# Kernel tuning notes

Hardware: AMD Instinct MI355X
Metric: run time of the kernel (lower is better)

## Reference

```python
import jax, jax.numpy as jnp
import numpy as np

D_MODEL = 256
D_INNER = 512
NHEADS = 8
HEADDIM = 64
NGROUPS = 1
D_DIST = 4
LOG_SCALE = 512.0
MAX_VALUE = 4.0
NUM_POINTS = 10
EPS = 1e-5


def roty(t):
    c, s = jnp.cos(t), jnp.sin(t)
    z, o = jnp.zeros_like(t), jnp.ones_like(t)
    r0 = jnp.stack([c, z, s], -1)
    r1 = jnp.stack([z, o, z], -1)
    r2 = jnp.stack([-s, z, c], -1)
    return jnp.stack([r0, r1, r2], -2)


def box_corners(center, size, angle):
    # flip_axis_to_camera: (x, -z, y)
    cam_c = jnp.stack([center[..., 0], -center[..., 2], center[..., 1]], -1)
    R = roty(angle)  # (B,K,3,3)
    sx = jnp.array([1, 1, -1, -1, 1, 1, -1, -1], jnp.float32)
    sy = jnp.array([1, 1, 1, 1, -1, -1, -1, -1], jnp.float32)
    sz = jnp.array([1, -1, -1, 1, 1, -1, -1, 1], jnp.float32)
    l, w, h = size[..., 0:1], size[..., 1:2], size[..., 2:3]
    local = jnp.stack([l * sx / 2, h * sy / 2, w * sz / 2], -1)  # (B,K,8,3)
    cam = jnp.einsum('bkcj,bkij->bkci', local, R) + cam_c[..., None, :]
    # camera -> lidar: (x, z, -y)
    return jnp.stack([cam[..., 0], cam[..., 2], -cam[..., 1]], -1)


def trilinear_sample(table, g):
    # table (P,P,P,C); g (N,3) normalized coords (gx,gy,gz); gx->axis2, gy->axis1, gz->axis0
    # replicates F.grid_sample(mode='bilinear', align_corners=False, padding_mode='zeros')
    P = table.shape[0]
    pix = ((g + 1.0) * P - 1.0) * 0.5
    k, j, i = pix[:, 0], pix[:, 1], pix[:, 2]
    i0f, j0f, k0f = jnp.floor(i), jnp.floor(j), jnp.floor(k)
    wi, wj, wk = i - i0f, j - j0f, k - k0f
    i0, j0, k0 = i0f.astype(jnp.int32), j0f.astype(jnp.int32), k0f.astype(jnp.int32)
    out = jnp.zeros((g.shape[0], table.shape[-1]), table.dtype)
    for a in (0, 1):
        for b in (0, 1):
            for c in (0, 1):
                ii, jj, kk = i0 + a, j0 + b, k0 + c
                valid = (ii >= 0) & (ii < P) & (jj >= 0) & (jj < P) & (kk >= 0) & (kk < P)
                v = table[jnp.clip(ii, 0, P - 1), jnp.clip(jj, 0, P - 1), jnp.clip(kk, 0, P - 1)]
                w = (wi if a else 1 - wi) * (wj if b else 1 - wj) * (wk if c else 1 - wk)
                out = out + jnp.where(valid, w, 0.0)[:, None] * v
    return out


def box_dist(key_xyz, query_xyz, query_size, query_angle, w1, b1, w2):
    B, K = query_xyz.shape[:2]
    L = key_xyz.shape[1]
    corners = jax.lax.stop_gradient(box_corners(query_xyz, query_size, query_angle))
    d = corners.reshape(B, K * 8, 3)[:, :, None, :] - key_xyz[:, None, :, :]  # (B,K*8,L,3)
    d = jnp.stack([d[..., 0], -d[..., 2], d[..., 1]], -1)
    R = roty(jnp.tile(query_angle, (1, 8)))  # matches torch .repeat((1,8)) ordering (bug-faithful)
    d = jnp.einsum('bqlj,bqjk->bqlk', d, R)
    d = jnp.stack([d[..., 0], d[..., 2], -d[..., 1]], -1)
    d = jnp.sign(d) * jnp.log2(jnp.abs(d) * LOG_SCALE + 1.0) / np.float32(np.log2(8.0))
    g = (d / MAX_VALUE).reshape(-1, 3)
    lin = jnp.linspace(-MAX_VALUE, MAX_VALUE, NUM_POINTS, dtype=jnp.float32)
    coords = jnp.stack(jnp.meshgrid(lin, lin, lin, indexing='ij'), -1)  # (P,P,P,3)
    table = jnp.maximum(coords @ w1.T + b1, 0.0) @ w2.T  # cpb MLP -> (P,P,P,4)
    samp = trilinear_sample(table, g).reshape(B, K, 8, L, D_DIST)
    return samp.sum(axis=2).transpose(0, 2, 1, 3)  # (B,L,K,4)


def dwconv7(x, w, b):
    # x (B,L,C), depthwise conv1d k=7 pad=3
    y = jax.lax.conv_general_dilated(jnp.swapaxes(x, 1, 2), w, (1,), [(3, 3)],
                                     dimension_numbers=('NCH', 'OIH', 'NCH'),
                                     feature_group_count=w.shape[0])
    return jnp.swapaxes(y + b[None, :, None], 1, 2)


def issm_scan(x, Bm, Cm, dt, A, h0):
    # x (B,L,H,hd), Bm/Cm (B,L,K), dt (B,L,K,H), h0 (B,H,hd,K); state index = query axis K
    dA = jnp.exp(dt * A)          # (B,L,K,H)
    dB = dt * Bm[..., None]       # (B,L,K,H)
    xs = (jnp.moveaxis(x, 1, 0), jnp.moveaxis(dA, 1, 0), jnp.moveaxis(dB, 1, 0), jnp.moveaxis(Cm, 1, 0))

    def step(h, inp):
        x_t, dA_t, dB_t, C_t = inp
        h = h * jnp.swapaxes(dA_t, 1, 2)[:, :, None, :] + x_t[..., None] * jnp.swapaxes(dB_t, 1, 2)[:, :, None, :]
        return h, jnp.einsum('bhdk,bk->bhd', h, C_t)

    hT, ys = jax.lax.scan(step, h0, xs)
    return jnp.moveaxis(ys, 0, 1), hT


def _forward(in_key, in_query, key_xyz, query_xyz, query_size, query_angle, Wkey, conv_w, conv_b, convb_w, convb_b, Wq, Wbc, Wdt, dt_bias, A_log, Dp, Wok, Woq, key_norm_w, ln_w, ln_b, cpb_w1, cpb_b1, cpb_w2):
    B, L, _ = in_key.shape
    K = in_query.shape[1]
    zxbcdt = in_key @ Wkey.T
    z = zxbcdt[..., :D_INNER]
    xbc = zxbcdt[..., D_INNER:2 * D_INNER + 2 * NGROUPS]
    dt_k = zxbcdt[..., 2 * D_INNER + 2 * NGROUPS:]
    xbc_f = jax.nn.silu(dwconv7(xbc, conv_w, conv_b))
    x = xbc_f[..., :D_INNER].reshape(B, L, NHEADS, HEADDIM)
    b_bias = xbc_f[..., D_INNER:D_INNER + NGROUPS]
    c_bias = xbc_f[..., D_INNER + NGROUPS:]
    xbc_b = jax.nn.silu(dwconv7(xbc_f, convb_w, convb_b))
    x_b = xbc_b[..., :D_INNER].reshape(B, L, NHEADS, HEADDIM)
    bb_b = xbc_b[..., D_INNER:D_INNER + NGROUPS]
    cb_b = xbc_b[..., D_INNER + NGROUPS:]
    dist = box_dist(key_xyz, query_xyz, query_size, query_angle, cpb_w1, cpb_b1, cpb_w2)  # (B,L,K,4)
    bc = dist @ Wbc.T  # (B,L,K,2*ngroups)
    Bm0, Cm0 = bc[..., 0], bc[..., 1]
    dt = jax.nn.softplus(dist @ Wdt.T + dt_k[:, :, None, :] + dt_bias)  # (B,L,K,H)
    A = -jnp.exp(A_log)
    h0 = (in_query @ Wq.T).reshape(B, K, NHEADS, HEADDIM).transpose(0, 2, 3, 1)  # (B,H,hd,K)
    y_f, h_f = issm_scan(x, Bm0 + b_bias, Cm0 + c_bias, dt, A, h0)
    rev = lambda a: jnp.flip(a, axis=1)
    y_b, h_b = issm_scan(rev(x_b), rev(Bm0 + bb_b), rev(Cm0 + cb_b), rev(dt), A, h0)
    y = y_f + rev(y_b) + Dp[None, None, :, None] * x
    yk = y.reshape(B, L, D_INNER)
    gated = yk * jax.nn.silu(z)
    gated = gated * jax.lax.rsqrt(jnp.mean(gated * gated, -1, keepdims=True) + EPS) * key_norm_w
    out_key = gated @ Wok.T
    state = (0.5 * (h_f + h_b)).transpose(0, 3, 1, 2).reshape(B, K, D_INNER)
    mu = jnp.mean(state, -1, keepdims=True)
    var = jnp.mean((state - mu) ** 2, -1, keepdims=True)
    out_query = (((state - mu) * jax.lax.rsqrt(var + EPS)) * ln_w + ln_b) @ Woq.T
    return out_key, out_query


def setup_inputs():
    key = jax.random.key(0)
    ks = jax.random.split(key, 24)
    B, L, K = 2, 1024, 128
    D, DI, H, G = D_MODEL, D_INNER, NHEADS, NGROUPS
    CC = DI + 2 * G
    n = jax.random.normal
    inp = {}
    inp['in_key'] = n(ks[0], (B, L, D), jnp.float32)
    inp['in_query'] = n(ks[1], (B, K, D), jnp.float32)
    inp['key_xyz'] = jax.random.uniform(ks[2], (B, L, 3))
    inp['query_xyz'] = jax.random.uniform(ks[3], (B, K, 3))
    inp['query_size'] = jax.random.uniform(ks[4], (B, K, 3)) + 0.1
    inp['query_angle'] = jax.random.uniform(ks[5], (B, K)) * 2.0 * np.float32(np.pi)
    inp['Wkey'] = n(ks[6], (2 * DI + 2 * G + H, D)) * 0.02
    inp['conv_w'] = n(ks[7], (CC, 1, 7)) * 0.1
    inp['conv_b'] = jnp.zeros((CC,))
    inp['convb_w'] = n(ks[8], (CC, 1, 7)) * 0.1
    inp['convb_b'] = jnp.zeros((CC,))
    inp['Wq'] = n(ks[9], (DI, D)) * 0.02
    inp['Wbc'] = n(ks[10], (2 * G, D_DIST)) * 0.1
    inp['Wdt'] = n(ks[11], (H, D_DIST)) * 0.1
    dt = jnp.exp(jax.random.uniform(ks[12], (H,)) * (np.float32(np.log(0.1)) - np.float32(np.log(1e-4))) + np.float32(np.log(1e-4)))
    inp['dt_bias'] = dt + jnp.log(-jnp.expm1(-dt))
    inp['A_log'] = jnp.log(jax.random.uniform(ks[13], (H,), minval=1.0, maxval=16.0))
    inp['Dp'] = jnp.ones((H,))
    inp['Wok'] = n(ks[14], (D, DI)) * 0.02
    inp['Woq'] = n(ks[15], (D, DI)) * 0.02
    inp['key_norm_w'] = jnp.ones((DI,))
    inp['ln_w'] = jnp.ones((DI,))
    inp['ln_b'] = jnp.zeros((DI,))
    inp['cpb_w1'] = n(ks[16], (128, 3)) * 0.1
    inp['cpb_b1'] = jnp.zeros((128,))
    inp['cpb_w2'] = n(ks[17], (D_DIST, 128)) * 0.1
    return inp


def reference(in_key, in_query, key_xyz, query_xyz, query_size, query_angle, Wkey, conv_w, conv_b, convb_w, convb_b, Wq, Wbc, Wdt, dt_bias, A_log, Dp, Wok, Woq, key_norm_w, ln_w, ln_b, cpb_w1, cpb_b1, cpb_w2):
    return _forward(in_key, in_query, key_xyz, query_xyz, query_size, query_angle, Wkey, conv_w, conv_b, convb_w, convb_b, Wq, Wbc, Wdt, dt_bias, A_log, Dp, Wok, Woq, key_norm_w, ln_w, ln_b, cpb_w1, cpb_b1, cpb_w2)
```

## Files before the change

kernel.cpp:

```cpp
#include <hip/hip_runtime.h>
#include <math.h>

#define B_ 2
#define L_ 1024
#define K_ 128
#define DM 256
#define DI 512
#define NH 8
#define HD 64
#define CC 514
#define ZCOLS 1034
#define NC 16
#define TC 64

typedef __attribute__((ext_vector_type(8))) short bf16x8;
typedef __attribute__((ext_vector_type(4))) float f32x4;

__device__ __forceinline__ float wave_sum(float v) {
    v += __shfl_xor(v, 1);  v += __shfl_xor(v, 2);  v += __shfl_xor(v, 4);
    v += __shfl_xor(v, 8);  v += __shfl_xor(v, 16); v += __shfl_xor(v, 32);
    return v;
}

__device__ __forceinline__ float dpp_row_reduce16(float v) {
    int t;
    t = __builtin_amdgcn_update_dpp(0, __float_as_int(v), 0x128, 0xF, 0xF, true);
    v += __int_as_float(t);
    t = __builtin_amdgcn_update_dpp(0, __float_as_int(v), 0x124, 0xF, 0xF, true);
    v += __int_as_float(t);
    t = __builtin_amdgcn_update_dpp(0, __float_as_int(v), 0x122, 0xF, 0xF, true);
    v += __int_as_float(t);
    t = __builtin_amdgcn_update_dpp(0, __float_as_int(v), 0x121, 0xF, 0xF, true);
    v += __int_as_float(t);
    return v;
}

__device__ __forceinline__ float silu_f(float x) {
    return x / (1.f + expf(-x));
}

__device__ __forceinline__ unsigned short f2bf(float f) {
    unsigned u = __float_as_uint(f);
    u = (u + 0x7FFFu + ((u >> 16) & 1u)) >> 16;
    return (unsigned short)u;
}

__global__ __launch_bounds__(256) void cvt_k(
    const float* __restrict__ ik, const float* __restrict__ wk,
    const float* __restrict__ iq, const float* __restrict__ wq,
    const float* __restrict__ wok,
    unsigned short* __restrict__ ikb, unsigned short* __restrict__ wkb,
    unsigned short* __restrict__ iqb, unsigned short* __restrict__ wqb,
    unsigned short* __restrict__ wokb) {
    int i = blockIdx.x * 256 + threadIdx.x;
    float4 v;
    ushort4* dst;
    if (i < 131072) {
        v = ((const float4*)ik)[i];
        dst = ((ushort4*)ikb) + i;
    } else if (i < 200704) {
        int j = i - 131072;
        v = (j < 66176) ? ((const float4*)wk)[j] : make_float4(0.f, 0.f, 0.f, 0.f);
        dst = ((ushort4*)wkb) + j;
    } else if (i < 217088) {
        int j = i - 200704;
        v = ((const float4*)iq)[j];
        dst = ((ushort4*)iqb) + j;
    } else if (i < 249856) {
        int j = i - 217088;
        v = ((const float4*)wq)[j];
        dst = ((ushort4*)wqb) + j;
    } else if (i < 282624) {
        int j = i - 249856;
        v = ((const float4*)wok)[j];
        dst = ((ushort4*)wokb) + j;
    } else return;
    ushort4 o;
    o.x = f2bf(v.x); o.y = f2bf(v.y); o.z = f2bf(v.z); o.w = f2bf(v.w);
    *dst = o;
}

__device__ __forceinline__ void mfma_dev(
    const unsigned short* __restrict__ A, const unsigned short* __restrict__ B,
    float* __restrict__ C, int ldc, int K, int bm, int bn, int nmax) {
    int tid = threadIdx.x;
    int lane = tid & 63, wv = tid >> 6;
    int wm = wv >> 1, wn = wv & 1;
    int r = lane & 15, kg = lane >> 4;
    const unsigned short* A0 = A + (size_t)(bm + wm * 32 + r) * K + kg * 8;
    const unsigned short* A1 = A0 + 16 * K;
    const unsigned short* B0 = B + (size_t)(bn + wn * 32 + r) * K + kg * 8;
    const unsigned short* B1 = B0 + 16 * K;
    f32x4 acc00 = {0.f, 0.f, 0.f, 0.f}, acc01 = acc00, acc10 = acc00, acc11 = acc00;
#pragma unroll 4
    for (int k0 = 0; k0 < K; k0 += 32) {
        bf16x8 a0 = *(const bf16x8*)(A0 + k0);
        bf16x8 a1 = *(const bf16x8*)(A1 + k0);
        bf16x8 b0 = *(const bf16x8*)(B0 + k0);
        bf16x8 b1 = *(const bf16x8*)(B1 + k0);
        acc00 = __builtin_amdgcn_mfma_f32_16x16x32_bf16(a0, b0, acc00, 0, 0, 0);
        acc01 = __builtin_amdgcn_mfma_f32_16x16x32_bf16(a0, b1, acc01, 0, 0, 0);
        acc10 = __builtin_amdgcn_mfma_f32_16x16x32_bf16(a1, b0, acc10, 0, 0, 0);
        acc11 = __builtin_amdgcn_mfma_f32_16x16x32_bf16(a1, b1, acc11, 0, 0, 0);
    }
    int mb = bm + wm * 32, nb = bn + wn * 32;
#pragma unroll
    for (int j = 0; j < 4; ++j) {
        int m0 = mb + kg * 4 + j;
        int n0 = nb + r;
        if (n0 < nmax)      C[(size_t)m0 * ldc + n0] = acc00[j];
        if (n0 + 16 < nmax) C[(size_t)m0 * ldc + n0 + 16] = acc01[j];
        int m1 = m0 + 16;
        if (n0 < nmax)      C[(size_t)m1 * ldc + n0] = acc10[j];
        if (n0 + 16 < nmax) C[(size_t)m1 * ldc + n0 + 16] = acc11[j];
    }
}

__global__ __launch_bounds__(256, 4) void front_k(
    const unsigned short* __restrict__ ikb, const unsigned short* __restrict__ wkb,
    const unsigned short* __restrict__ iqb, const unsigned short* __restrict__ wqb,
    const float* __restrict__ in_key, const float* __restrict__ Wkey,
    float* __restrict__ zx, float* __restrict__ h0b,
    const float* __restrict__ qxyz, const float* __restrict__ qsize,
    const float* __restrict__ qang, const float* __restrict__ w1,
    const float* __restrict__ b1, const float* __restrict__ w2,
    float* __restrict__ cb, float* __restrict__ tbl) {
    int bid = blockIdx.x, tid = threadIdx.x;
    if (bid < 544) {
        mfma_dev(ikb, wkb, zx, ZCOLS, 256, (bid & 31) * 64, (bid >> 5) * 64, 1026);
    } else if (bid < 576) {
        int rr = bid - 544;
        mfma_dev(iqb, wqb, h0b, 512, 256, (rr & 3) * 64, (rr >> 2) * 64, 512);
    } else if (bid < 584) {
        int idx = (bid - 576) * 256 + tid;
        int b = idx >> 10;
        int q = idx & 1023;
        int k = q >> 3;
        int c = q & 7;
        const float sx[8] = {1, 1, -1, -1, 1, 1, -1, -1};
        const float sy[8] = {1, 1, 1, 1, -1, -1, -1, -1};
        const float sz[8] = {1, -1, -1, 1, 1, -1, -1, 1};
        float cx = qxyz[(b * K_ + k) * 3 + 0];
        float cy = qxyz[(b * K_ + k) * 3 + 1];
        float cz = qxyz[(b * K_ + k) * 3 + 2];
        float lv = qsize[(b * K_ + k) * 3 + 0];
        float wv2 = qsize[(b * K_ + k) * 3 + 1];
        float hv = qsize[(b * K_ + k) * 3 + 2];
        float ang = qang[b * K_ + k];
        float ca = cosf(ang), sa = sinf(ang);
        float ccx = cx, ccy = -cz, ccz = cy;
        float l0 = lv * sx[c] * 0.5f;
        float l1 = hv * sy[c] * 0.5f;
        float l2 = wv2 * sz[c] * 0.5f;
        float m0 = ca * l0 + sa * l2 + ccx;
        float m1 = l1 + ccy;
        float m2 = -sa * l0 + ca * l2 + ccz;
        float angr = qang[b * K_ + (q & (K_ - 1))];
        float4* o = (float4*)(cb + (size_t)idx * 8);
        o[0] = make_float4(m0, m2, -m1, cosf(angr));
        o[1] = make_float4(sinf(angr), 0.f, 0.f, 0.f);
    } else if (bid < 588) {
        int p = (bid - 584) * 256 + tid;
        if (p >= 1000) return;
        int i = p / 100, j = (p / 10) % 10, k = p % 10;
        float c0 = (8.f / 9.f) * i - 4.f;
        float c1 = (8.f / 9.f) * j - 4.f;
        float c2 = (8.f / 9.f) * k - 4.f;
        float a0 = 0.f, a1 = 0.f, a2 = 0.f, a3 = 0.f;
        for (int m = 0; m < 128; ++m) {
            float t = fmaf(c0, w1[m * 3 + 0], fmaf(c1, w1[m * 3 + 1], fmaf(c2, w1[m * 3 + 2], b1[m])));
            t = fmaxf(t, 0.f);
            a0 = fmaf(t, w2[m], a0);
            a1 = fmaf(t, w2[128 + m], a1);
            a2 = fmaf(t, w2[256 + m], a2);
            a3 = fmaf(t, w2[384 + m], a3);
        }
        tbl[p * 4 + 0] = a0; tbl[p * 4 + 1] = a1;
        tbl[p * 4 + 2] = a2; tbl[p * 4 + 3] = a3;
    } else {
        int row = (bid - 588) * 32 + (tid >> 3);
        int colh = tid & 7;
        const float* arow = in_key + (size_t)row * 256;
        const float* wrow = Wkey + (size_t)(1026 + colh) * 256;
        float acc = 0.f;
#pragma unroll 8
        for (int k = 0; k < 256; k += 4) {
            float4 a = *(const float4*)(arow + k);
            float4 wv2 = *(const float4*)(wrow + k);
            acc = fmaf(a.x, wv2.x, fmaf(a.y, wv2.y, fmaf(a.z, wv2.z, fmaf(a.w, wv2.w, acc))));
        }
        zx[(size_t)row * ZCOLS + 1026 + colh] = acc;
    }
}

__global__ void dwconv_silu(const float* __restrict__ xin, int in_stride, int in_off,
                            const float* __restrict__ w, const float* __restrict__ bias,
                            float* __restrict__ out) {
    int c = blockIdx.y * blockDim.x + threadIdx.x;
    if (c >= CC) return;
    int row0 = blockIdx.x * 2;
    int l0 = row0 & (L_ - 1);
    const float* xr = xin + (size_t)row0 * in_stride + in_off + c;
    float Lv[8];
#pragma unroll
    for (int i = 0; i < 8; ++i) {
        int ll = l0 + i - 3;
        Lv[i] = (ll >= 0 && ll < L_) ? xr[(ptrdiff_t)(i - 3) * in_stride] : 0.f;
    }
    float acc0 = bias[c], acc1 = bias[c];
#pragma unroll
    for (int j = 0; j < 7; ++j) {
        float wj = w[c * 7 + j];
        acc0 = fmaf(Lv[j], wj, acc0);
        acc1 = fmaf(Lv[j + 1], wj, acc1);
    }
    out[(size_t)row0 * CC + c] = silu_f(acc0);
    out[(size_t)(row0 + 1) * CC + c] = silu_f(acc1);
}

__global__ __launch_bounds__(128) void geo_k(
    const float* __restrict__ kxyz, const float* __restrict__ cb,
    const float* __restrict__ tbl, const float* __restrict__ zx,
    const float* __restrict__ xf, const float* __restrict__ xb,
    const float* __restrict__ wbc, const float* __restrict__ wdt,
    const float* __restrict__ dtb, const float* __restrict__ alog,
    float* __restrict__ dA, float* __restrict__ dBf, float* __restrict__ dBb,
    float* __restrict__ Cf, float* __restrict__ Cb) {
    __shared__ float t_s[4000];
    int row = blockIdx.x;
    int b = row >> 10;
    int l = row & 1023;
    int k = threadIdx.x;
    for (int i = threadIdx.x; i < 4000; i += 128) t_s[i] = tbl[i];
    __syncthreads();
    float kx = kxyz[(size_t)row * 3 + 0];
    float ky = kxyz[(size_t)row * 3 + 1];
    float kz = kxyz[(size_t)row * 3 + 2];
    float acc0 = 0.f, acc1 = 0.f, acc2 = 0.f, acc3 = 0.f;
#pragma unroll
    for (int c = 0; c < 8; ++c) {
        int q = k * 8 + c;
        const float4* p = (const float4*)(cb + (size_t)(b * 1024 + q) * 8);
        float4 v0 = p[0], v1 = p[1];
        float d0 = v0.x - kx, d1 = v0.y - ky, d2 = v0.z - kz;
        float rc = v0.w, rs = v1.x;
        float e0 = d0, e1 = -d2, e2 = d1;
        float f0 = rc * e0 - rs * e2;
        float f1 = e1;
        float f2 = rs * e0 + rc * e2;
        float g0 = f0, g1 = f2, g2 = -f1;
        g0 = copysignf(log2f(fabsf(g0) * 512.f + 1.f) * (1.f / 12.f), g0);
        g1 = copysignf(log2f(fabsf(g1) * 512.f + 1.f) * (1.f / 12.f), g1);
        g2 = copysignf(log2f(fabsf(g2) * 512.f + 1.f) * (1.f / 12.f), g2);
        float iq = 5.f * g2 + 4.5f;
        float jq = 5.f * g1 + 4.5f;
        float kq = 5.f * g0 + 4.5f;
        float i0f = floorf(iq), j0f = floorf(jq), k0f = floorf(kq);
        float wi = iq - i0f, wj = jq - j0f, wk = kq - k0f;
        int i0 = (int)i0f, j0 = (int)j0f, k0 = (int)k0f;
#pragma unroll
        for (int a = 0; a < 2; ++a) {
#pragma unroll
            for (int bb = 0; bb < 2; ++bb) {
#pragma unroll
                for (int cc = 0; cc < 2; ++cc) {
                    int ii = i0 + a, jj = j0 + bb, kk = k0 + cc;
                    if ((unsigned)ii < 10u && (unsigned)jj < 10u && (unsigned)kk < 10u) {
                        float wgt = (a ? wi : 1.f - wi) * (bb ? wj : 1.f - wj) * (cc ? wk : 1.f - wk);
                        const float* tp = &t_s[((ii * 10 + jj) * 10 + kk) * 4];
                        acc0 = fmaf(wgt, tp[0], acc0);
                        acc1 = fmaf(wgt, tp[1], acc1);
                        acc2 = fmaf(wgt, tp[2], acc2);
                        acc3 = fmaf(wgt, tp[3], acc3);
                    }
                }
            }
        }
    }
    float B0 = acc0 * wbc[0] + acc1 * wbc[1] + acc2 * wbc[2] + acc3 * wbc[3];
    float C0 = acc0 * wbc[4] + acc1 * wbc[5] + acc2 * wbc[6] + acc3 * wbc[7];
    float bbf = xf[(size_t)row * CC + 512], cbf = xf[(size_t)row * CC + 513];
    float bbb = xb[(size_t)row * CC + 512], cbb = xb[(size_t)row * CC + 513];
    Cf[(size_t)row * K_ + k] = C0 + cbf;
    Cb[(size_t)row * K_ + k] = C0 + cbb;
    float Bf = B0 + bbf, Bb = B0 + bbb;
#pragma unroll
    for (int hh = 0; hh < NH; ++hh) {
        float s = acc0 * wdt[hh * 4 + 0] + acc1 * wdt[hh * 4 + 1] +
                  acc2 * wdt[hh * 4 + 2] + acc3 * wdt[hh * 4 + 3];
        s += zx[(size_t)row * ZCOLS + 1026 + hh] + dtb[hh];
        float dtv = (s > 20.f) ? s : log1pf(expf(s));
        float Av = -expf(alog[hh]);
        size_t o = ((size_t)(b * NH + hh) * L_ + l) * K_ + k;
        dA[o] = expf(dtv * Av);
        dBf[o] = dtv * Bf;
        dBb[o] = dtv * Bb;
    }
}

__global__ __launch_bounds__(256) void scan_part6(
    const float* __restrict__ dA, const float* __restrict__ dBf, const float* __restrict__ dBb,
    const float* __restrict__ Cf, const float* __restrict__ Cb,
    const float* __restrict__ xf, const float* __restrict__ xb,
    float* __restrict__ Sbuf, float* __restrict__ Pbuf,
    float* __restrict__ yf, float* __restrict__ yb) {
    __shared__ float lds[2][3584];
    int bid = blockIdx.x;
    int c = bid & 15;
    int hh = (bid >> 4) & 7;
    int b = (bid >> 7) & 1;
    int dir = bid >> 8;
    int tid = threadIdx.x;
    int lane = tid & 63;
    int w = tid >> 6;
    int dg = lane >> 4, kg = lane & 15;
    int dloc = w * 4 + dg;
    int klo = kg * 4, khi = 64 + kg * 4;

    const float* Bsrc = dir ? dBb : dBf;
    const float* Csrc = dir ? Cb : Cf;
    const float* Xsrc = dir ? xb : xf;
    float* Ydst = dir ? yb : yf;
    int t0 = dir ? (L_ - 1 - c * TC) : c * TC;
    int stp = dir ? -1 : 1;

    const float* Abase = dA + ((size_t)(b * NH + hh) * L_) * K_;
    const float* Bbase = Bsrc + ((size_t)(b * NH + hh) * L_) * K_;
    const float* Cbase = Csrc + ((size_t)b * L_) * K_;
    const float* Xbase = Xsrc + ((size_t)b * L_) * CC + hh * HD;

    const bool hasx = (tid < 128);

    auto gaddr = [&](int v, int tb) -> const float* {
        if (v < 768) {
            int r = (v >> 5) & 7;
            int c4 = v & 31;
            int l = t0 + stp * (tb + r);
            const float* base = (v < 256) ? Abase : ((v < 512) ? Bbase : Cbase);
            return base + (size_t)l * K_ + c4 * 4;
        } else {
            int vv = v - 768;
            int r = vv >> 4, c4 = vv & 15;
            int l = t0 + stp * (tb + r);
            return Xbase + (size_t)l * CC + c4 * 4;
        }
    };

    float hA[8] = {0, 0, 0, 0, 0, 0, 0, 0};
    float hB[8] = {0, 0, 0, 0, 0, 0, 0, 0};
    float hC[8] = {0, 0, 0, 0, 0, 0, 0, 0};
    float hD[8] = {0, 0, 0, 0, 0, 0, 0, 0};
    float cum[8] = {1, 1, 1, 1, 1, 1, 1, 1};

    float4 rA = *(const float4*)gaddr(tid, 0);
    float4 rB = *(const float4*)gaddr(256 + tid, 0);
    float4 rC = *(const float4*)gaddr(512 + tid, 0);
    float4 rX = hasx ? *(const float4*)gaddr(768 + tid, 0) : make_float4(0, 0, 0, 0);
    *(float4*)&lds[0][4 * tid] = rA;
    *(float4*)&lds[0][1024 + 4 * tid] = rB;
    *(float4*)&lds[0][2048 + 4 * tid] = rC;
    if (hasx) *(float4*)&lds[0][3072 + 4 * tid] = rX;
    __syncthreads();

    float* pY = Ydst + ((size_t)(b * L_ + t0)) * DI + hh * HD + dloc;
    const ptrdiff_t dY = (ptrdiff_t)stp * DI;

    for (int it = 0; it < TC / 8; ++it) {
        int tb = it * 8;
        if (it < TC / 8 - 1) {
            rA = *(const float4*)gaddr(tid, tb + 8);
            rB = *(const float4*)gaddr(256 + tid, tb + 8);
            rC = *(const float4*)gaddr(512 + tid, tb + 8);
            if (hasx) rX = *(const float4*)gaddr(768 + tid, tb + 8);
        }
        const float* Lb = lds[it & 1];
        float4 aC0 = *(const float4*)&Lb[klo];
        float4 aC1 = *(const float4*)&Lb[khi];
        float4 bC0 = *(const float4*)&Lb[1024 + klo];
        float4 bC1 = *(const float4*)&Lb[1024 + khi];
        float4 cC0 = *(const float4*)&Lb[2048 + klo];
        float4 cC1 = *(const float4*)&Lb[2048 + khi];
        float x0 = Lb[3072 + dloc];
        float x1 = Lb[3072 + 16 + dloc];
        float x2 = Lb[3072 + 32 + dloc];
        float x3 = Lb[3072 + 48 + dloc];
        float4 aN0 = *(const float4*)&Lb[128 + klo];
        float4 aN1 = *(const float4*)&Lb[128 + khi];
        float4 bN0 = *(const float4*)&Lb[1024 + 128 + klo];
        float4 bN1 = *(const float4*)&Lb[1024 + 128 + khi];
#pragma unroll
        for (int st = 0; st < 8; ++st) {
            float4 aF0, aF1, bF0, bF1, cN0, cN1;
            float nx0 = 0.f, nx1 = 0.f, nx2 = 0.f, nx3 = 0.f;
            if (st < 6) {
                int o = (st + 2) * 128;
                aF0 = *(const float4*)&Lb[o + klo];
                aF1 = *(const float4*)&Lb[o + khi];
                bF0 = *(const float4*)&Lb[1024 + o + klo];
                bF1 = *(const float4*)&Lb[1024 + o + khi];
            }
            if (st < 7) {
                int o = (st + 1) * 128;
                cN0 = *(const float4*)&Lb[2048 + o + klo];
                cN1 = *(const float4*)&Lb[2048 + o + khi];
                int xo = 3072 + (st + 1) * 64 + dloc;
                nx0 = Lb[xo]; nx1 = Lb[xo + 16]; nx2 = Lb[xo + 32]; nx3 = Lb[xo + 48];
            }
            cum[0] *= aC0.x; cum[1] *= aC0.y; cum[2] *= aC0.z; cum[3] *= aC0.w;
            cum[4] *= aC1.x; cum[5] *= aC1.y; cum[6] *= aC1.z; cum[7] *= aC1.w;
            float u0, u1, u2, u3;
            hA[0] = fmaf(hA[0], aC0.x, x0 * bC0.x); u0 = hA[0] * cC0.x;
            hA[1] = fmaf(hA[1], aC0.y, x0 * bC0.y); u1 = hA[1] * cC0.y;
            hA[2] = fmaf(hA[2], aC0.z, x0 * bC0.z); u2 = hA[2] * cC0.z;
            hA[3] = fmaf(hA[3], aC0.w, x0 * bC0.w); u3 = hA[3] * cC0.w;
            hA[4] = fmaf(hA[4], aC1.x, x0 * bC1.x); u0 = fmaf(hA[4], cC1.x, u0);
            hA[5] = fmaf(hA[5], aC1.y, x0 * bC1.y); u1 = fmaf(hA[5], cC1.y, u1);
            hA[6] = fmaf(hA[6], aC1.z, x0 * bC1.z); u2 = fmaf(hA[6], cC1.z, u2);
            hA[7] = fmaf(hA[7], aC1.w, x0 * bC1.w); u3 = fmaf(hA[7], cC1.w, u3);
            float rrA = dpp_row_reduce16((u0 + u1) + (u2 + u3));
            hB[0] = fmaf(hB[0], aC0.x, x1 * bC0.x); u0 = hB[0] * cC0.x;
            hB[1] = fmaf(hB[1], aC0.y, x1 * bC0.y); u1 = hB[1] * cC0.y;
            hB[2] = fmaf(hB[2], aC0.z, x1 * bC0.z); u2 = hB[2] * cC0.z;
            hB[3] = fmaf(hB[3], aC0.w, x1 * bC0.w); u3 = hB[3] * cC0.w;
            hB[4] = fmaf(hB[4], aC1.x, x1 * bC1.x); u0 = fmaf(hB[4], cC1.x, u0);
            hB[5] = fmaf(hB[5], aC1.y, x1 * bC1.y); u1 = fmaf(hB[5], cC1.y, u1);
            hB[6] = fmaf(hB[6], aC1.z, x1 * bC1.z); u2 = fmaf(hB[6], cC1.z, u2);
            hB[7] = fmaf(hB[7], aC1.w, x1 * bC1.w); u3 = fmaf(hB[7], cC1.w, u3);
            float rrB = dpp_row_reduce16((u0 + u1) + (u2 + u3));
            hC[0] = fmaf(hC[0], aC0.x, x2 * bC0.x); u0 = hC[0] * cC0.x;
            hC[1] = fmaf(hC[1], aC0.y, x2 * bC0.y); u1 = hC[1] * cC0.y;
            hC[2] = fmaf(hC[2], aC0.z, x2 * bC0.z); u2 = hC[2] * cC0.z;
            hC[3] = fmaf(hC[3], aC0.w, x2 * bC0.w); u3 = hC[3] * cC0.w;
            hC[4] = fmaf(hC[4], aC1.x, x2 * bC1.x); u0 = fmaf(hC[4], cC1.x, u0);
            hC[5] = fmaf(hC[5], aC1.y, x2 * bC1.y); u1 = fmaf(hC[5], cC1.y, u1);
            hC[6] = fmaf(hC[6], aC1.z, x2 * bC1.z); u2 = fmaf(hC[6], cC1.z, u2);
            hC[7] = fmaf(hC[7], aC1.w, x2 * bC1.w); u3 = fmaf(hC[7], cC1.w, u3);
            float rrC = dpp_row_reduce16((u0 + u1) + (u2 + u3));
            hD[0] = fmaf(hD[0], aC0.x, x3 * bC0.x); u0 = hD[0] * cC0.x;
            hD[1] = fmaf(hD[1], aC0.y, x3 * bC0.y); u1 = hD[1] * cC0.y;
            hD[2] = fmaf(hD[2], aC0.z, x3 * bC0.z); u2 = hD[2] * cC0.z;
            hD[3] = fmaf(hD[3], aC0.w, x3 * bC0.w); u3 = hD[3] * cC0.w;
            hD[4] = fmaf(hD[4], aC1.x, x3 * bC1.x); u0 = fmaf(hD[4], cC1.x, u0);
            hD[5] = fmaf(hD[5], aC1.y, x3 * bC1.y); u1 = fmaf(hD[5], cC1.y, u1);
            hD[6] = fmaf(hD[6], aC1.z, x3 * bC1.z); u2 = fmaf(hD[6], cC1.z, u2);
            hD[7] = fmaf(hD[7], aC1.w, x3 * bC1.w); u3 = fmaf(hD[7], cC1.w, u3);
            float rrD = dpp_row_reduce16((u0 + u1) + (u2 + u3));
            if (kg == 0) { pY[0] = rrA; pY[16] = rrB; pY[32] = rrC; pY[48] = rrD; }
            pY += dY;
            if (st < 7) {
                aC0 = aN0; aC1 = aN1; bC0 = bN0; bC1 = bN1;
                cC0 = cN0; cC1 = cN1;
                x0 = nx0; x1 = nx1; x2 = nx2; x3 = nx3;
                if (st < 6) { aN0 = aF0; aN1 = aF1; bN0 = bF0; bN1 = bF1; }
            }
        }
        if (it < TC / 8 - 1) {
            *(float4*)&lds[(it + 1) & 1][4 * tid] = rA;
            *(float4*)&lds[(it + 1) & 1][1024 + 4 * tid] = rB;
            *(float4*)&lds[(it + 1) & 1][2048 + 4 * tid] = rC;
            if (hasx) *(float4*)&lds[(it + 1) & 1][3072 + 4 * tid] = rX;
        }
        __syncthreads();
    }

    int ibh = (dir * B_ + b) * NH + hh;
    {
        float* Sp = Sbuf + (((size_t)ibh * NC + c) * HD + dloc) * K_;
        *(float4*)(Sp + klo) = make_float4(hA[0], hA[1], hA[2], hA[3]);
        *(float4*)(Sp + khi) = make_float4(hA[4], hA[5], hA[6], hA[7]);
        Sp += (size_t)16 * K_;
        *(float4*)(Sp + klo) = make_float4(hB[0], hB[1], hB[2], hB[3]);
        *(float4*)(Sp + khi) = make_float4(hB[4], hB[5], hB[6], hB[7]);
        Sp += (size_t)16 * K_;
        *(float4*)(Sp + klo) = make_float4(hC[0], hC[1], hC[2], hC[3]);
        *(float4*)(Sp + khi) = make_float4(hC[4], hC[5], hC[6], hC[7]);
        Sp += (size_t)16 * K_;
        *(float4*)(Sp + klo) = make_float4(hD[0], hD[1], hD[2], hD[3]);
        *(float4*)(Sp + khi) = make_float4(hD[4], hD[5], hD[6], hD[7]);
    }
    if (dir == 0 && tid < 16) {
        float* Pp = Pbuf + ((size_t)((b * NH + hh) * NC + c)) * K_;
        *(float4*)(Pp + klo) = make_float4(cum[0], cum[1], cum[2], cum[3]);
        *(float4*)(Pp + khi) = make_float4(cum[4], cum[5], cum[6], cum[7]);
    }
}

__global__ __launch_bounds__(256) void scan_combine(
    const float* __restrict__ h0buf, float* __restrict__ Sbuf,
    const float* __restrict__ Pbuf, float* __restrict__ hfin) {
    int bid = blockIdx.x;
    int dq = bid & 3;
    int hh = (bid >> 2) & 7;
    int b = (bid >> 5) & 1;
    int dir = bid >> 6;
    int tid = threadIdx.x;
    int w = tid >> 6;
    int lane = tid & 63;
    int dsl = dq * 4 + w;
    int dg = lane >> 4, kg = lane & 15;
    int d = dsl * 4 + dg;
    int k0 = kg * 8;

    float H[8];
#pragma unroll
    for (int j = 0; j < 8; ++j)
        H[j] = h0buf[(size_t)(b * K_ + k0 + j) * DI + hh * HD + d];

    int ibh = (dir * B_ + b) * NH + hh;
    for (int c = 0; c < NC; ++c) {
        float* Sp = Sbuf + (((size_t)ibh * NC + c) * HD + d) * K_ + k0;
        int cF = dir ? (NC - 1 - c) : c;
        const float* Pp = Pbuf + ((size_t)((b * NH + hh) * NC + cF)) * K_ + k0;
        float4 sA = *(const float4*)(Sp + 0);
        float4 sB = *(const float4*)(Sp + 4);
        float4 pA = *(const float4*)(Pp + 0);
        float4 pB = *(const float4*)(Pp + 4);
        *(float4*)(Sp + 0) = make_float4(H[0], H[1], H[2], H[3]);
        *(float4*)(Sp + 4) = make_float4(H[4], H[5], H[6], H[7]);
        H[0] = fmaf(H[0], pA.x, sA.x); H[1] = fmaf(H[1], pA.y, sA.y);
        H[2] = fmaf(H[2], pA.z, sA.z); H[3] = fmaf(H[3], pA.w, sA.w);
        H[4] = fmaf(H[4], pB.x, sB.x); H[5] = fmaf(H[5], pB.y, sB.y);
        H[6] = fmaf(H[6], pB.z, sB.z); H[7] = fmaf(H[7], pB.w, sB.w);
    }
    float* hf = hfin + ((((size_t)dir * B_ + b) * NH + hh) * HD + d) * K_ + k0;
    *(float4*)(hf + 0) = make_float4(H[0], H[1], H[2], H[3]);
    *(float4*)(hf + 4) = make_float4(H[4], H[5], H[6], H[7]);
}

#define CP 72
#define WSWZ(k) ((((k) >> 3) & 3) << 2)
__global__ __launch_bounds__(256) void scan_corr(
    const float* __restrict__ dA, const float* __restrict__ Cf, const float* __restrict__ Cb,
    const float* __restrict__ Sbuf, float* __restrict__ yf, float* __restrict__ yb) {
    __shared__ float Wl[128][CP];
    __shared__ float Hl[128][CP];
    int iid = blockIdx.x;
    int c = iid & 15;
    int hh = (iid >> 4) & 7;
    int b = (iid >> 7) & 1;
    int dir = iid >> 8;
    int tid = threadIdx.x;
    const float* Csrc = dir ? Cb : Cf;

    if (tid < 128) {
        int k = tid;
        float cum = 1.f;
        const float* pA = dA + ((size_t)(b * NH + hh) * L_) * K_ + k;
        const float* pC = Csrc + ((size_t)b * L_) * K_ + k;
        int sw = WSWZ(k);
#pragma unroll 4
        for (int t = 0; t < TC; ++t) {
            int l = dir ? (L_ - 1 - (c * TC + t)) : (c * TC + t);
            cum *= pA[(size_t)l * K_];
            Wl[k][t ^ sw] = cum * pC[(size_t)l * K_];
        }
    }
    {
        int d = tid & 63, kq = tid >> 6;
        int ibh = (dir * B_ + b) * NH + hh;
        const float* Hp = Sbuf + (((size_t)ibh * NC + c) * HD + d) * K_;
#pragma unroll
        for (int i = 0; i < 8; ++i) {
            int q = kq * 8 + i;
            float4 v = *(const float4*)(Hp + q * 4);
            Hl[q * 4 + 0][d] = v.x; Hl[q * 4 + 1][d] = v.y;
            Hl[q * 4 + 2][d] = v.z; Hl[q * 4 + 3][d] = v.w;
        }
    }
    __syncthreads();
    int a = tid >> 4;
    int bc = tid & 15;
    int t0v = a * 4, d0v = bc * 4;
    float acc[4][4] = {};
    for (int k = 0; k < 128; ++k) {
        float4 w4 = *(const float4*)&Wl[k][t0v ^ WSWZ(k)];
        float4 h4 = *(const float4*)&Hl[k][d0v];
        acc[0][0] = fmaf(w4.x, h4.x, acc[0][0]); acc[0][1] = fmaf(w4.x, h4.y, acc[0][1]);
        acc[0][2] = fmaf(w4.x, h4.z, acc[0][2]); acc[0][3] = fmaf(w4.x, h4.w, acc[0][3]);
        acc[1][0] = fmaf(w4.y, h4.x, acc[1][0]); acc[1][1] = fmaf(w4.y, h4.y, acc[1][1]);
        acc[1][2] = fmaf(w4.y, h4.z, acc[1][2]); acc[1][3] = fmaf(w4.y, h4.w, acc[1][3]);
        acc[2][0] = fmaf(w4.z, h4.x, acc[2][0]); acc[2][1] = fmaf(w4.z, h4.y, acc[2][1]);
        acc[2][2] = fmaf(w4.z, h4.z, acc[2][2]); acc[2][3] = fmaf(w4.z, h4.w, acc[2][3]);
        acc[3][0] = fmaf(w4.w, h4.x, acc[3][0]); acc[3][1] = fmaf(w4.w, h4.y, acc[3][1]);
        acc[3][2] = fmaf(w4.w, h4.z, acc[3][2]); acc[3][3] = fmaf(w4.w, h4.w, acc[3][3]);
    }
    float* Ydst = dir ? yb : yf;
#pragma unroll
    for (int i = 0; i < 4; ++i) {
        int t = t0v + i;
        int l = dir ? (L_ - 1 - (c * TC + t)) : (c * TC + t);
        float* yp = Ydst + ((size_t)(b * L_ + l)) * DI + hh * HD + d0v;
        float4 old = *(float4*)yp;
        old.x += acc[i][0]; old.y += acc[i][1];
        old.z += acc[i][2]; old.w += acc[i][3];
        *(float4*)yp = old;
    }
}

__global__ __launch_bounds__(256) void gated_k(
    const float* __restrict__ yf, const float* __restrict__ yb,
    const float* __restrict__ xf, const float* __restrict__ zx,
    const float* __restrict__ Dp, const float* __restrict__ knw,
    unsigned short* __restrict__ gatedb) {
    __shared__ float sb[4];
    int row = blockIdx.x;
    int tid = threadIdx.x;
    float g[2];
    float ss = 0.f;
#pragma unroll
    for (int u = 0; u < 2; ++u) {
        int c = tid + u * 256;
        float yv = yf[(size_t)row * DI + c] + yb[(size_t)row * DI + c] +
                   Dp[c >> 6] * xf[(size_t)row * CC + c];
        float z = zx[(size_t)row * ZCOLS + c];
        float gv = yv * silu_f(z);
        g[u] = gv;
        ss = fmaf(gv, gv, ss);
    }
    float wsum = wave_sum(ss);
    if ((tid & 63) == 0) sb[tid >> 6] = wsum;
    __syncthreads();
    float tot = sb[0] + sb[1] + sb[2] + sb[3];
    float rms = rsqrtf(tot * (1.f / 512.f) + 1e-5f);
#pragma unroll
    for (int u = 0; u < 2; ++u) {
        int c = tid + u * 256;
        gatedb[(size_t)row * DI + c] = f2bf(g[u] * rms * knw[c]);
    }
}

__global__ __launch_bounds__(256) void final_k(
    const unsigned short* __restrict__ gatedb, const unsigned short* __restrict__ wokb,
    float* __restrict__ out,
    const float* __restrict__ hfin, const float* __restrict__ lnw,
    const float* __restrict__ lnb, const float* __restrict__ woq,
    float* __restrict__ outq) {
    int bid = blockIdx.x, tid = threadIdx.x;
    if (bid < 128) {
        mfma_dev(gatedb, wokb, out, 256, 512, (bid & 31) * 64, (bid >> 5) * 64, 256);
        return;
    }
    __shared__ float sln[512];
    __shared__ float sb1[4];
    __shared__ float sb2[4];
    int bk = bid - 128;
    int b = bk >> 7;
    int k = bk & 127;
    float st[2];
    float ssum = 0.f;
#pragma unroll
    for (int u = 0; u < 2; ++u) {
        int c = tid + u * 256;
        int hh = c >> 6, d = c & 63;
        size_t o0 = (((size_t)(0 * B_ + b) * NH + hh) * HD + d) * K_ + k;
        size_t o1 = (((size_t)(1 * B_ + b) * NH + hh) * HD + d) * K_ + k;
        st[u] = 0.5f * (hfin[o0] + hfin[o1]);
        ssum += st[u];
    }
    float wsum = wave_sum(ssum);
    if ((tid & 63) == 0) sb1[tid >> 6] = wsum;
    __syncthreads();
    float mu = (sb1[0] + sb1[1] + sb1[2] + sb1[3]) * (1.f / 512.f);
    float vs = 0.f;
#pragma unroll
    for (int u = 0; u < 2; ++u) {
        float t = st[u] - mu;
        vs = fmaf(t, t, vs);
    }
    float wv = wave_sum(vs);
    if ((tid & 63) == 0) sb2[tid >> 6] = wv;
    __syncthreads();
    float var = (sb2[0] + sb2[1] + sb2[2] + sb2[3]) * (1.f / 512.f);
    float inv = rsqrtf(var + 1e-5f);
#pragma unroll
    for (int u = 0; u < 2; ++u) {
        int c = tid + u * 256;
        sln[c] = (st[u] - mu) * inv * lnw[c] + lnb[c];
    }
    __syncthreads();
    const float4* w4 = (const float4*)(woq + (size_t)tid * 512);
    float acc = 0.f;
#pragma unroll 4
    for (int i = 0; i < 128; ++i) {
        float4 wvv = w4[i];
        float4 sv = *(const float4*)&sln[i * 4];
        acc = fmaf(wvv.x, sv.x, acc);
        acc = fmaf(wvv.y, sv.y, acc);
        acc = fmaf(wvv.z, sv.z, acc);
        acc = fmaf(wvv.w, sv.w, acc);
    }
    outq[(size_t)bk * 256 + tid] = acc;
}

extern "C" void kernel_launch(void* const* d_in, const int* in_sizes, int n_in,
                              void* d_out, int out_size, void* d_ws, size_t ws_size,
                              hipStream_t stream) {
    const float* in_key      = (const float*)d_in[0];
    const float* in_query    = (const float*)d_in[1];
    const float* key_xyz     = (const float*)d_in[2];
    const float* query_xyz   = (const float*)d_in[3];
    const float* query_size  = (const float*)d_in[4];
    const float* query_angle = (const float*)d_in[5];
    const float* Wkey        = (const float*)d_in[6];
    const float* conv_w      = (const float*)d_in[7];
    const float* conv_b      = (const float*)d_in[8];
    const float* convb_w     = (const float*)d_in[9];
    const float* convb_b     = (const float*)d_in[10];
    const float* Wq          = (const float*)d_in[11];
    const float* Wbc         = (const float*)d_in[12];
    const float* Wdt         = (const float*)d_in[13];
    const float* dt_bias     = (const float*)d_in[14];
    const float* A_log       = (const float*)d_in[15];
    const float* Dp          = (const float*)d_in[16];
    const float* Wok         = (const float*)d_in[17];
    const float* Woq         = (const float*)d_in[18];
    const float* key_norm_w  = (const float*)d_in[19];
    const float* ln_w        = (const float*)d_in[20];
    const float* ln_b        = (const float*)d_in[21];
    const float* cpb_w1      = (const float*)d_in[22];
    const float* cpb_b1      = (const float*)d_in[23];
    const float* cpb_w2      = (const float*)d_in[24];
    float* out = (float*)d_out;

    float* wsf = (float*)d_ws;
    float* zx    = wsf + 0;
    float* xf    = wsf + 2117632;
    float* xb    = wsf + 3170304;
    float* tbl   = wsf + 4222976;
    float* cbuf  = wsf + 4226976;
    float* Pbuf  = wsf + 4243360;
    float* dAa   = wsf + 5291936;
    float* dBf   = wsf + 7389088;
    float* dBb   = wsf + 9486240;
    float* Cfb   = wsf + 11583392;
    float* Cbb   = wsf + 11845536;
    float* h0b   = wsf + 12107680;
    float* yfb   = wsf + 12238752;
    float* ybb   = wsf + 13287328;
    float* hfin  = wsf + 14335904;
    float* Sbuf  = wsf + 15646624;
    unsigned short* ikb    = (unsigned short*)(wsf + 19840928);
    unsigned short* wkb    = (unsigned short*)(wsf + 20103072);
    unsigned short* iqb    = (unsigned short*)(wsf + 20242336);
    unsigned short* wqb    = (unsigned short*)(wsf + 20275104);
    unsigned short* wokb   = (unsigned short*)(wsf + 20340640);
    unsigned short* gatedb = (unsigned short*)(wsf + 20406176);

    cvt_k<<<1104, 256, 0, stream>>>(in_key, Wkey, in_query, Wq, Wok,
                                    ikb, wkb, iqb, wqb, wokb);
    front_k<<<652, 256, 0, stream>>>(ikb, wkb, iqb, wqb, in_key, Wkey, zx, h0b,
                                     query_xyz, query_size, query_angle,
                                     cpb_w1, cpb_b1, cpb_w2, cbuf, tbl);
    dwconv_silu<<<dim3(1024, 3), 256, 0, stream>>>(zx, ZCOLS, 512, conv_w, conv_b, xf);
    dwconv_silu<<<dim3(1024, 3), 256, 0, stream>>>(xf, CC, 0, convb_w, convb_b, xb);
    geo_k<<<2048, 128, 0, stream>>>(key_xyz, cbuf, tbl, zx, xf, xb,
                                    Wbc, Wdt, dt_bias, A_log,
                                    dAa, dBf, dBb, Cfb, Cbb);
    scan_part6<<<512, 256, 0, stream>>>(dAa, dBf, dBb, Cfb, Cbb, xf, xb,
                                        Sbuf, Pbuf, yfb, ybb);
    scan_combine<<<128, 256, 0, stream>>>(h0b, Sbuf, Pbuf, hfin);
    scan_corr<<<512, 256, 0, stream>>>(dAa, Cfb, Cbb, Sbuf, yfb, ybb);
    gated_k<<<2048, 256, 0, stream>>>(yfb, ybb, xf, zx, Dp, key_norm_w, gatedb);
    final_k<<<384, 256, 0, stream>>>(gatedb, wokb, out, hfin, ln_w, ln_b, Woq,
                                     out + 524288);
}
```

Baseline: 164.4 us.

## Fuse bf16 conversion into MFMA loads and merge backward conv with geometry kernel

Removes the separate fp32-to-bf16 conversion kernel: the GEMM now loads fp32 operands and converts them to bf16 in registers, with row guards for the padded weight. The backward depthwise conv is merged into the geometry kernel launch, which also recomputes the two B/C columns locally. The gating/norm stage now writes fp32 and runs alongside the query projection, with the output GEMM split into its own kernel. Launch count drops, but the GEMMs now read twice as many bytes and redo the conversion in every tile.

```diff
diff --git a/kernel.cpp b/kernel.cpp
--- a/kernel.cpp
+++ b/kernel.cpp
@@ -45,59 +45,38 @@
     return (unsigned short)u;
 }
 
-__global__ __launch_bounds__(256) void cvt_k(
-    const float* __restrict__ ik, const float* __restrict__ wk,
-    const float* __restrict__ iq, const float* __restrict__ wq,
-    const float* __restrict__ wok,
-    unsigned short* __restrict__ ikb, unsigned short* __restrict__ wkb,
-    unsigned short* __restrict__ iqb, unsigned short* __restrict__ wqb,
-    unsigned short* __restrict__ wokb) {
-    int i = blockIdx.x * 256 + threadIdx.x;
-    float4 v;
-    ushort4* dst;
-    if (i < 131072) {
-        v = ((const float4*)ik)[i];
-        dst = ((ushort4*)ikb) + i;
-    } else if (i < 200704) {
-        int j = i - 131072;
-        v = (j < 66176) ? ((const float4*)wk)[j] : make_float4(0.f, 0.f, 0.f, 0.f);
-        dst = ((ushort4*)wkb) + j;
-    } else if (i < 217088) {
-        int j = i - 200704;
-        v = ((const float4*)iq)[j];
-        dst = ((ushort4*)iqb) + j;
-    } else if (i < 249856) {
-        int j = i - 217088;
-        v = ((const float4*)wq)[j];
-        dst = ((ushort4*)wqb) + j;
-    } else if (i < 282624) {
-        int j = i - 249856;
-        v = ((const float4*)wok)[j];
-        dst = ((ushort4*)wokb) + j;
-    } else return;
-    ushort4 o;
-    o.x = f2bf(v.x); o.y = f2bf(v.y); o.z = f2bf(v.z); o.w = f2bf(v.w);
-    *dst = o;
+__device__ __forceinline__ bf16x8 ld_cvt8(const float* p) {
+    float4 v0 = *(const float4*)p;
+    float4 v1 = *(const float4*)(p + 4);
+    bf16x8 r;
+    r[0] = (short)f2bf(v0.x); r[1] = (short)f2bf(v0.y);
+    r[2] = (short)f2bf(v0.z); r[3] = (short)f2bf(v0.w);
+    r[4] = (short)f2bf(v1.x); r[5] = (short)f2bf(v1.y);
+    r[6] = (short)f2bf(v1.z); r[7] = (short)f2bf(v1.w);
+    return r;
 }
 
 __device__ __forceinline__ void mfma_dev(
-    const unsigned short* __restrict__ A, const unsigned short* __restrict__ B,
-    float* __restrict__ C, int ldc, int K, int bm, int bn, int nmax) {
+    const float* __restrict__ A, const float* __restrict__ B,
+    float* __restrict__ C, int ldc, int K, int bm, int bn, int nmax, int Brows) {
     int tid = threadIdx.x;
     int lane = tid & 63, wv = tid >> 6;
     int wm = wv >> 1, wn = wv & 1;
     int r = lane & 15, kg = lane >> 4;
-    const unsigned short* A0 = A + (size_t)(bm + wm * 32 + r) * K + kg * 8;
-    const unsigned short* A1 = A0 + 16 * K;
-    const unsigned short* B0 = B + (size_t)(bn + wn * 32 + r) * K + kg * 8;
-    const unsigned short* B1 = B0 + 16 * K;
+    const float* A0 = A + (size_t)(bm + wm * 32 + r) * K + kg * 8;
+    const float* A1 = A0 + 16 * K;
+    int br0 = bn + wn * 32 + r, br1 = br0 + 16;
+    bool bv0 = br0 < Brows, bv1 = br1 < Brows;
+    const float* B0 = B + (size_t)(bv0 ? br0 : 0) * K + kg * 8;
+    const float* B1 = B + (size_t)(bv1 ? br1 : 0) * K + kg * 8;
     f32x4 acc00 = {0.f, 0.f, 0.f, 0.f}, acc01 = acc00, acc10 = acc00, acc11 = acc00;
+    bf16x8 z8 = {};
 #pragma unroll 4
     for (int k0 = 0; k0 < K; k0 += 32) {
-        bf16x8 a0 = *(const bf16x8*)(A0 + k0);
-        bf16x8 a1 = *(const bf16x8*)(A1 + k0);
-        bf16x8 b0 = *(const bf16x8*)(B0 + k0);
-        bf16x8 b1 = *(const bf16x8*)(B1 + k0);
+        bf16x8 a0 = ld_cvt8(A0 + k0);
+        bf16x8 a1 = ld_cvt8(A1 + k0);
+        bf16x8 b0 = ld_cvt8(B0 + k0); if (!bv0) b0 = z8;
+        bf16x8 b1 = ld_cvt8(B1 + k0); if (!bv1) b1 = z8;
         acc00 = __builtin_amdgcn_mfma_f32_16x16x32_bf16(a0, b0, acc00, 0, 0, 0);
         acc01 = __builtin_amdgcn_mfma_f32_16x16x32_bf16(a0, b1, acc01, 0, 0, 0);
         acc10 = __builtin_amdgcn_mfma_f32_16x16x32_bf16(a1, b0, acc10, 0, 0, 0);
@@ -116,21 +95,21 @@
     }
 }
 
-__global__ __launch_bounds__(256, 4) void front_k(
-    const unsigned short* __restrict__ ikb, const unsigned short* __restrict__ wkb,
-    const unsigned short* __restrict__ iqb, const unsigned short* __restrict__ wqb,
+__global__ __launch_bounds__(256) void front_k(
     const float* __restrict__ in_key, const float* __restrict__ Wkey,
-    float* __restrict__ zx, float* __restrict__ h0b,
+    float* __restrict__ zx,
+    const float* __restrict__ in_query, const float* __restrict__ Wq,
+    float* __restrict__ h0b,
     const float* __restrict__ qxyz, const float* __restrict__ qsize,
     const float* __restrict__ qang, const float* __restrict__ w1,
     const float* __restrict__ b1, const float* __restrict__ w2,
     float* __restrict__ cb, float* __restrict__ tbl) {
     int bid = blockIdx.x, tid = threadIdx.x;
     if (bid < 544) {
-        mfma_dev(ikb, wkb, zx, ZCOLS, 256, (bid & 31) * 64, (bid >> 5) * 64, 1026);
+        mfma_dev(in_key, Wkey, zx, ZCOLS, 256, (bid & 31) * 64, (bid >> 5) * 64, 1026, ZCOLS);
     } else if (bid < 576) {
         int rr = bid - 544;
-        mfma_dev(iqb, wqb, h0b, 512, 256, (rr & 3) * 64, (rr >> 2) * 64, 512);
+        mfma_dev(in_query, Wq, h0b, 512, 256, (rr & 3) * 64, (rr >> 2) * 64, 512, 512);
     } else if (bid < 584) {
         int idx = (bid - 576) * 256 + tid;
         int b = idx >> 10;
@@ -218,20 +197,60 @@
     out[(size_t)(row0 + 1) * CC + c] = silu_f(acc1);
 }
 
-__global__ __launch_bounds__(128) void geo_k(
-    const float* __restrict__ kxyz, const float* __restrict__ cb,
+__global__ __launch_bounds__(256) void mid_k(
+    const float* __restrict__ xf, const float* __restrict__ convb_w,
+    const float* __restrict__ convb_b, float* __restrict__ xb,
+    const float* __restrict__ kxyz, const float* __restrict__ cbuf,
     const float* __restrict__ tbl, const float* __restrict__ zx,
-    const float* __restrict__ xf, const float* __restrict__ xb,
     const float* __restrict__ wbc, const float* __restrict__ wdt,
     const float* __restrict__ dtb, const float* __restrict__ alog,
     float* __restrict__ dA, float* __restrict__ dBf, float* __restrict__ dBb,
     float* __restrict__ Cf, float* __restrict__ Cb) {
+    int bid = blockIdx.x, tid = threadIdx.x;
+    if (bid < 3072) {
+        int crange = bid % 3;
+        int c = crange * 256 + tid;
+        if (c >= CC) return;
+        int row0 = (bid / 3) * 2;
+        int l0 = row0 & (L_ - 1);
+        const float* xr = xf + (size_t)row0 * CC + c;
+        float Lv[8];
+#pragma unroll
+        for (int i = 0; i < 8; ++i) {
+            int ll = l0 + i - 3;
+            Lv[i] = (ll >= 0 && ll < L_) ? xr[(ptrdiff_t)(i - 3) * CC] : 0.f;
+        }
+        float acc0 = convb_b[c], acc1 = convb_b[c];
+#pragma unroll
+        for (int j = 0; j < 7; ++j) {
+            float wj = convb_w[c * 7 + j];
+            acc0 = fmaf(Lv[j], wj, acc0);
+            acc1 = fmaf(Lv[j + 1], wj, acc1);
+        }
+        xb[(size_t)row0 * CC + c] = silu_f(acc0);
+        xb[(size_t)(row0 + 1) * CC + c] = silu_f(acc1);
+        return;
+    }
     __shared__ float t_s[4000];
-    int row = blockIdx.x;
+    __shared__ float bcs[2][2];
+    int gid = bid - 3072;
+    int half = tid >> 7;
+    int k = tid & 127;
+    int row = gid * 2 + half;
     int b = row >> 10;
     int l = row & 1023;
-    int k = threadIdx.x;
-    for (int i = threadIdx.x; i < 4000; i += 128) t_s[i] = tbl[i];
+    for (int i = tid; i < 4000; i += 256) t_s[i] = tbl[i];
+    if (k < 2) {
+        int c = 512 + k;
+        const float* xr = xf + (size_t)row * CC + c;
+        float acc = convb_b[c];
+#pragma unroll
+        for (int j = 0; j < 7; ++j) {
+            int ll = l + j - 3;
+            if (ll >= 0 && ll < L_) acc = fmaf(xr[(ptrdiff_t)(j - 3) * CC], convb_w[c * 7 + j], acc);
+        }
+        bcs[half][k] = silu_f(acc);
+    }
     __syncthreads();
     float kx = kxyz[(size_t)row * 3 + 0];
     float ky = kxyz[(size_t)row * 3 + 1];
@@ -240,7 +259,7 @@
 #pragma unroll
     for (int c = 0; c < 8; ++c) {
         int q = k * 8 + c;
-        const float4* p = (const float4*)(cb + (size_t)(b * 1024 + q) * 8);
+        const float4* p = (const float4*)(cbuf + (size_t)(b * 1024 + q) * 8);
         float4 v0 = p[0], v1 = p[1];
         float d0 = v0.x - kx, d1 = v0.y - ky, d2 = v0.z - kz;
         float rc = v0.w, rs = v1.x;
@@ -280,7 +299,7 @@
     float B0 = acc0 * wbc[0] + acc1 * wbc[1] + acc2 * wbc[2] + acc3 * wbc[3];
     float C0 = acc0 * wbc[4] + acc1 * wbc[5] + acc2 * wbc[6] + acc3 * wbc[7];
     float bbf = xf[(size_t)row * CC + 512], cbf = xf[(size_t)row * CC + 513];
-    float bbb = xb[(size_t)row * CC + 512], cbb = xb[(size_t)row * CC + 513];
+    float bbb = bcs[half][0], cbb = bcs[half][1];
     Cf[(size_t)row * K_ + k] = C0 + cbf;
     Cb[(size_t)row * K_ + k] = C0 + cbb;
     float Bf = B0 + bbf, Bb = B0 + bbb;
@@ -597,53 +616,46 @@
     }
 }
 
-__global__ __launch_bounds__(256) void gated_k(
+__global__ __launch_bounds__(256) void gatedq_k(
     const float* __restrict__ yf, const float* __restrict__ yb,
     const float* __restrict__ xf, const float* __restrict__ zx,
     const float* __restrict__ Dp, const float* __restrict__ knw,
-    unsigned short* __restrict__ gatedb) {
-    __shared__ float sb[4];
-    int row = blockIdx.x;
-    int tid = threadIdx.x;
-    float g[2];
-    float ss = 0.f;
-#pragma unroll
-    for (int u = 0; u < 2; ++u) {
-        int c = tid + u * 256;
-        float yv = yf[(size_t)row * DI + c] + yb[(size_t)row * DI + c] +
-                   Dp[c >> 6] * xf[(size_t)row * CC + c];
-        float z = zx[(size_t)row * ZCOLS + c];
-        float gv = yv * silu_f(z);
-        g[u] = gv;
-        ss = fmaf(gv, gv, ss);
-    }
-    float wsum = wave_sum(ss);
-    if ((tid & 63) == 0) sb[tid >> 6] = wsum;
-    __syncthreads();
-    float tot = sb[0] + sb[1] + sb[2] + sb[3];
-    float rms = rsqrtf(tot * (1.f / 512.f) + 1e-5f);
-#pragma unroll
-    for (int u = 0; u < 2; ++u) {
-        int c = tid + u * 256;
-        gatedb[(size_t)row * DI + c] = f2bf(g[u] * rms * knw[c]);
-    }
-}
-
-__global__ __launch_bounds__(256) void final_k(
-    const unsigned short* __restrict__ gatedb, const unsigned short* __restrict__ wokb,
-    float* __restrict__ out,
+    float* __restrict__ gated,
     const float* __restrict__ hfin, const float* __restrict__ lnw,
     const float* __restrict__ lnb, const float* __restrict__ woq,
     float* __restrict__ outq) {
     int bid = blockIdx.x, tid = threadIdx.x;
-    if (bid < 128) {
-        mfma_dev(gatedb, wokb, out, 256, 512, (bid & 31) * 64, (bid >> 5) * 64, 256);
+    if (bid < 2048) {
+        __shared__ float sb[4];
+        int row = bid;
+        float g[2];
+        float ss = 0.f;
+#pragma unroll
+        for (int u = 0; u < 2; ++u) {
+            int c = tid + u * 256;
+            float yv = yf[(size_t)row * DI + c] + yb[(size_t)row * DI + c] +
+                       Dp[c >> 6] * xf[(size_t)row * CC + c];
+            float z = zx[(size_t)row * ZCOLS + c];
+            float gv = yv * silu_f(z);
+            g[u] = gv;
+            ss = fmaf(gv, gv, ss);
+        }
+        float wsum = wave_sum(ss);
+        if ((tid & 63) == 0) sb[tid >> 6] = wsum;
+        __syncthreads();
+        float tot = sb[0] + sb[1] + sb[2] + sb[3];
+        float rms = rsqrtf(tot * (1.f / 512.f) + 1e-5f);
+#pragma unroll
+        for (int u = 0; u < 2; ++u) {
+            int c = tid + u * 256;
+            gated[(size_t)row * DI + c] = g[u] * rms * knw[c];
+        }
         return;
     }
     __shared__ float sln[512];
     __shared__ float sb1[4];
     __shared__ float sb2[4];
-    int bk = bid - 128;
+    int bk = bid - 2048;
     int b = bk >> 7;
     int k = bk & 127;
     float st[2];
@@ -690,6 +702,13 @@
         acc = fmaf(wvv.w, sv.w, acc);
     }
     outq[(size_t)bk * 256 + tid] = acc;
+}
+
+__global__ __launch_bounds__(256) void final_k(
+    const float* __restrict__ gated, const float* __restrict__ Wok,
+    float* __restrict__ out) {
+    int bid = blockIdx.x;
+    mfma_dev(gated, Wok, out, 256, 512, (bid & 31) * 64, (bid >> 5) * 64, 256, 256);
 }
 
 extern "C" void kernel_launch(void* const* d_in, const int* in_sizes, int n_in,
@@ -738,29 +757,22 @@
     float* yfb   = wsf + 12238752;
     float* ybb   = wsf + 13287328;
     float* hfin  = wsf + 14335904;
+    float* gated = wsf + 14598048;
     float* Sbuf  = wsf + 15646624;
-    unsigned short* ikb    = (unsigned short*)(wsf + 19840928);
-    unsigned short* wkb    = (unsigned short*)(wsf + 20103072);
-    unsigned short* iqb    = (unsigned short*)(wsf + 20242336);
-    unsigned short* wqb    = (unsigned short*)(wsf + 20275104);
-    unsigned short* wokb   = (unsigned short*)(wsf + 20340640);
-    unsigned short* gatedb = (unsigned short*)(wsf + 20406176);
-
-    cvt_k<<<1104, 256, 0, stream>>>(in_key, Wkey, in_query, Wq, Wok,
-                                    ikb, wkb, iqb, wqb, wokb);
-    front_k<<<652, 256, 0, stream>>>(ikb, wkb, iqb, wqb, in_key, Wkey, zx, h0b,
+
+    front_k<<<652, 256, 0, stream>>>(in_key, Wkey, zx, in_query, Wq, h0b,
                                      query_xyz, query_size, query_angle,
                                      cpb_w1, cpb_b1, cpb_w2, cbuf, tbl);
     dwconv_silu<<<dim3(1024, 3), 256, 0, stream>>>(zx, ZCOLS, 512, conv_w, conv_b, xf);
-    dwconv_silu<<<dim3(1024, 3), 256, 0, stream>>>(xf, CC, 0, convb_w, convb_b, xb);
-    geo_k<<<2048, 128, 0, stream>>>(key_xyz, cbuf, tbl, zx, xf, xb,
+    mid_k<<<4096, 256, 0, stream>>>(xf, convb_w, convb_b, xb,
+                                    key_xyz, cbuf, tbl, zx,
                                     Wbc, Wdt, dt_bias, A_log,
                                     dAa, dBf, dBb, Cfb, Cbb);
     scan_part6<<<512, 256, 0, stream>>>(dAa, dBf, dBb, Cfb, Cbb, xf, xb,
                                         Sbuf, Pbuf, yfb, ybb);
     scan_combine<<<128, 256, 0, stream>>>(h0b, Sbuf, Pbuf, hfin);
     scan_corr<<<512, 256, 0, stream>>>(dAa, Cfb, Cbb, Sbuf, yfb, ybb);
-    gated_k<<<2048, 256, 0, stream>>>(yfb, ybb, xf, zx, Dp, key_norm_w, gatedb);
-    final_k<<<384, 256, 0, stream>>>(gatedb, wokb, out, hfin, ln_w, ln_b, Woq,
-                                     out + 524288);
-}
+    gatedq_k<<<2304, 256, 0, stream>>>(yfb, ybb, xf, zx, Dp, key_norm_w, gated,
+                                       hfin, ln_w, ln_b, Woq, out + 524288);
+    final_k<<<128, 256, 0, stream>>>(gated, Wok, out);
+}
```

After: 240.0 us. 1.46x slower.
